# Kernel optimization log

Hardware: AMD Instinct MI355X
Metric: run time of the kernel (lower is better)

Reference implementation:

```python
import jax, jax.numpy as jnp
import numpy as np

B, T, D = 2, 2048, 2048
H = 8
DK = 256   # head_qk_dim
DV = 512   # head_v_dim
C = 64     # retention chunk size
EPS = 1e-5
ROPE_BASE = 10000.0


def _rotary(x):
    # x: [B, T, H, DK], non-interleaved (rotate-half) rotary over full head dim
    half = DK // 2
    inv_freq = 1.0 / (ROPE_BASE ** (jnp.arange(0, DK, 2, dtype=jnp.float32) / DK))
    freqs = jnp.arange(T, dtype=jnp.float32)[:, None] * inv_freq[None, :]  # [T, half]
    cos = jnp.cos(freqs)[None, :, None, :].astype(x.dtype)
    sin = jnp.sin(freqs)[None, :, None, :].astype(x.dtype)
    x1, x2 = x[..., :half], x[..., half:]
    return jnp.concatenate([x1 * cos - x2 * sin, x2 * cos + x1 * sin], axis=-1)


def setup_inputs() -> dict:
    key = jax.random.key(0)
    ks = jax.random.split(key, 6)
    s = 2.0 ** (-2.5) * (2.0 / 2048.0) ** 0.5  # xavier_uniform-ish scale, gain 2^-2.5
    return {
        "hidden_states": jax.random.normal(ks[0], (B, T, D), jnp.float32),
        "Wq": jax.random.normal(ks[1], (H * DK, D), jnp.float32) * s,
        "Wk": jax.random.normal(ks[2], (H * DK, D), jnp.float32) * s,
        "Wv": jax.random.normal(ks[3], (H * DV, D), jnp.float32) * s,
        "Wg": jax.random.normal(ks[4], (H * DV, D), jnp.float32) * s,
        "Wo": jax.random.normal(ks[5], (D, H * DV), jnp.float32) * s,
        "g_norm_weight": jnp.ones((DV,), jnp.float32),
    }


def reference(hidden_states, Wq, Wk, Wv, Wg, Wo, g_norm_weight):
    x = hidden_states  # [B, T, D]
    q = (x @ Wq.T).reshape(B, T, H, DK)
    k = (x @ Wk.T).reshape(B, T, H, DK)
    q = _rotary(q)
    k = _rotary(k)
    q = q.transpose(0, 2, 1, 3) * (DK ** -0.5)        # [B, H, T, DK]
    k = k.transpose(0, 2, 1, 3)                       # [B, H, T, DK]
    v = (x @ Wv.T).reshape(B, T, H, DV).transpose(0, 2, 1, 3)  # [B, H, T, DV]

    # RetNet multi-scale per-head decay
    logb = jnp.log(1.0 - 2.0 ** (-5.0 - jnp.arange(H, dtype=jnp.float32)))  # [H]
    i = jnp.arange(C, dtype=jnp.float32)
    # intra-chunk decay mask b^{i-j} for i>=j: [H, C, C]
    Dmask = jnp.where(i[:, None] >= i[None, :],
                      jnp.exp(logb[:, None, None] * (i[:, None] - i[None, :])), 0.0)
    q_dec = jnp.exp(logb[:, None] * (i + 1.0))        # [H, C]  decay applied to q vs carried state
    k_dec = jnp.exp(logb[:, None] * (C - 1.0 - i))    # [H, C]  decay applied to k for state update
    chunk_dec = jnp.exp(logb * C)                     # [H]

    N = T // C
    qc = q.reshape(B, H, N, C, DK).transpose(2, 0, 1, 3, 4)  # [N, B, H, C, DK]
    kc = k.reshape(B, H, N, C, DK).transpose(2, 0, 1, 3, 4)
    vc = v.reshape(B, H, N, C, DV).transpose(2, 0, 1, 3, 4)

    def body(S, inp):
        qi, ki, vi = inp  # [B,H,C,DK], [B,H,C,DK], [B,H,C,DV]
        inter = jnp.einsum('bhcd,bhdv->bhcv', qi * q_dec[None, :, :, None], S)
        scores = jnp.einsum('bhcd,bhmd->bhcm', qi, ki) * Dmask[None]
        o = inter + jnp.einsum('bhcm,bhmv->bhcv', scores, vi)
        S_new = S * chunk_dec[None, :, None, None] + \
                jnp.einsum('bhcd,bhcv->bhdv', ki * k_dec[None, :, :, None], vi)
        return S_new, o

    S0 = jnp.zeros((B, H, DK, DV), x.dtype)
    _, oc = jax.lax.scan(body, S0, (qc, kc, vc))  # oc: [N, B, H, C, DV]
    o = oc.transpose(1, 2, 0, 3, 4).reshape(B, H, T, DV).transpose(0, 2, 1, 3)  # [B, T, H, DV]

    g = (x @ Wg.T).reshape(B, T, H, DV)
    # fused RMSNorm + swish gate (per head_v_dim)
    o_n = o * jax.lax.rsqrt(jnp.mean(o * o, axis=-1, keepdims=True) + EPS) * g_norm_weight
    o = o_n * (g * jax.nn.sigmoid(g))
    return o.reshape(B, T, H * DV) @ Wo.T  # [B, T, D]
```

## Files before the change

### kernel.cpp

```cpp
#include <hip/hip_runtime.h>


typedef unsigned short u16;
typedef unsigned int u32;
typedef short bf16x8 __attribute__((ext_vector_type(8)));
typedef short s16x4 __attribute__((ext_vector_type(4)));
typedef float f32x4 __attribute__((ext_vector_type(4)));
typedef u32 u32x2 __attribute__((ext_vector_type(2)));
typedef u32 u32x4 __attribute__((ext_vector_type(4)));

typedef __attribute__((address_space(3))) u32 lds_u32;
typedef __attribute__((address_space(1))) const u32 gbl_u32;

__device__ __forceinline__ float bf2f(u16 u) {
    union { u32 i; float f; } x; x.i = ((u32)u) << 16; return x.f;
}
__device__ __forceinline__ u16 f2bf(float f) {
    union { float f; u32 i; } x; x.f = f;
    u32 u = x.i;
    u += 0x7fffu + ((u >> 16) & 1u);
    return (u16)(u >> 16);
}
__device__ __forceinline__ f32x4 mfma16(bf16x8 a, bf16x8 b, f32x4 c) {
    return __builtin_amdgcn_mfma_f32_16x16x32_bf16(a, b, c, 0, 0, 0);
}
__device__ __forceinline__ void gload16(const u16* g, u16* lds) {
    __builtin_amdgcn_global_load_lds((gbl_u32*)(unsigned long long)g,
                                     (lds_u32*)(u32)(unsigned long long)lds, 16, 0, 0);
}

__global__ __launch_bounds__(256)
void cvt_bf16(const float* __restrict__ src, u16* __restrict__ dst)
{
    size_t i = ((size_t)blockIdx.x * 256 + threadIdx.x) * 8;
    f32x4 a = *(const f32x4*)(src + i);
    f32x4 b = *(const f32x4*)(src + i + 4);
    bf16x8 r;
#pragma unroll
    for (int j = 0; j < 4; j++) { r[j] = (short)f2bf(a[j]); r[j + 4] = (short)f2bf(b[j]); }
    *(bf16x8*)(dst + i) = r;
}

template<bool CF32>
__global__ __launch_bounds__(256, 2)
void gemm_bt(const u16* __restrict__ A, const u16* __restrict__ Bm,
             void* __restrict__ Cv, int N, int K)
{
    __shared__ u16 Ab[128 * 64];
    __shared__ u16 Bb[128 * 64];
    const int tid = threadIdx.x;
    const int lane = tid & 63, wave = tid >> 6;
    const int quad = lane >> 4, l16 = lane & 15;
    const int tn = blockIdx.x, tm = blockIdx.y;
    const int wr = wave >> 1, wc = wave & 1;

    f32x4 acc[4][4];
#pragma unroll
    for (int i = 0; i < 4; i++)
#pragma unroll
        for (int j = 0; j < 4; j++) acc[i][j] = (f32x4){0.f, 0.f, 0.f, 0.f};

    const u16* Abase = A + (size_t)tm * 128 * K;
    const u16* Bbase = Bm + (size_t)tn * 128 * K;
    const int rsub = lane >> 3, csub = (lane & 7) * 8;

    for (int k0 = 0; k0 < K; k0 += 64) {
        __syncthreads();
#pragma unroll
        for (int i = 0; i < 4; i++) {
            int chunk = wave * 4 + i;
            int r = chunk * 8 + rsub;
            gload16(Abase + (size_t)r * K + k0 + csub, Ab + chunk * 512);
            gload16(Bbase + (size_t)r * K + k0 + csub, Bb + chunk * 512);
        }
        __syncthreads();
#pragma unroll
        for (int kc = 0; kc < 2; kc++) {
            bf16x8 af[4], bfr[4];
#pragma unroll
            for (int mt = 0; mt < 4; mt++)
                af[mt] = *(const bf16x8*)(Ab + (wr * 64 + mt * 16 + l16) * 64 + kc * 32 + quad * 8);
#pragma unroll
            for (int nt = 0; nt < 4; nt++)
                bfr[nt] = *(const bf16x8*)(Bb + (wc * 64 + nt * 16 + l16) * 64 + kc * 32 + quad * 8);
#pragma unroll
            for (int mt = 0; mt < 4; mt++)
#pragma unroll
                for (int nt = 0; nt < 4; nt++)
                    acc[mt][nt] = mfma16(af[mt], bfr[nt], acc[mt][nt]);
        }
    }
    const int row0 = tm * 128 + wr * 64 + quad * 4;
    const int col0 = tn * 128 + wc * 64 + l16;
#pragma unroll
    for (int mt = 0; mt < 4; mt++)
#pragma unroll
        for (int nt = 0; nt < 4; nt++)
#pragma unroll
            for (int r = 0; r < 4; r++) {
                size_t idx = (size_t)(row0 + mt * 16 + r) * N + col0 + nt * 16;
                if constexpr (CF32) ((float*)Cv)[idx] = acc[mt][nt][r];
                else                ((u16*)Cv)[idx]   = f2bf(acc[mt][nt][r]);
            }
}

__global__ __launch_bounds__(256, 2)
void rotary_scores(u16* __restrict__ q, const u16* __restrict__ k,
                   u16* __restrict__ kT, u16* __restrict__ P)
{
    __shared__ u16 qS[64 * 264];
    __shared__ u16 kS[64 * 264];
    const int tid = threadIdx.x;
    const int lane = tid & 63, wave = tid >> 6;
    const int quad = lane >> 4, l16 = lane & 15;
    const int bx = blockIdx.x;
    const int bh = bx & 15, n = bx >> 4;
    const int b = bh >> 3, h = bh & 7;
    const int t0 = n * 64;

    const int row = tid >> 2;
    const int j0 = (tid & 3) * 32;
    const size_t rowbase = (size_t)(b * 2048 + t0 + row) * 2048 + h * 256;
    const float tpos = (float)(t0 + row);
#pragma unroll
    for (int i = 0; i < 4; i++) {
        int j = j0 + i * 8;
        bf16x8 x1 = *(const bf16x8*)(q + rowbase + j);
        bf16x8 x2 = *(const bf16x8*)(q + rowbase + j + 128);
        bf16x8 y1 = *(const bf16x8*)(k + rowbase + j);
        bf16x8 y2 = *(const bf16x8*)(k + rowbase + j + 128);
        bf16x8 o1, o2, p1, p2;
#pragma unroll
        for (int e = 0; e < 8; e++) {
            float inv = expf((-9.210340371976184f / 128.f) * (float)(j + e));
            float ang = tpos * inv;
            float sv = sinf(ang), cv = cosf(ang);
            float a = bf2f((u16)x1[e]), bb = bf2f((u16)x2[e]);
            o1[e] = (short)f2bf((a * cv - bb * sv) * 0.0625f);
            o2[e] = (short)f2bf((bb * cv + a * sv) * 0.0625f);
            float e1 = bf2f((u16)y1[e]), e2 = bf2f((u16)y2[e]);
            p1[e] = (short)f2bf(e1 * cv - e2 * sv);
            p2[e] = (short)f2bf(e2 * cv + e1 * sv);
        }
        *(bf16x8*)(q + rowbase + j)       = o1;
        *(bf16x8*)(q + rowbase + j + 128) = o2;
        *(bf16x8*)(qS + row * 264 + j)       = o1;
        *(bf16x8*)(qS + row * 264 + j + 128) = o2;
        *(bf16x8*)(kS + row * 264 + j)       = p1;
        *(bf16x8*)(kS + row * 264 + j + 128) = p2;
    }
    __syncthreads();

    const float logb = logf(1.0f - exp2f(-5.0f - (float)h));
    f32x4 sc[4];
#pragma unroll
    for (int i = 0; i < 4; i++) sc[i] = (f32x4){0.f, 0.f, 0.f, 0.f};
#pragma unroll
    for (int kc = 0; kc < 8; kc++) {
        bf16x8 af = *(const bf16x8*)(qS + (wave * 16 + l16) * 264 + kc * 32 + quad * 8);
#pragma unroll
        for (int mt = 0; mt < 4; mt++) {
            bf16x8 bk = *(const bf16x8*)(kS + (mt * 16 + l16) * 264 + kc * 32 + quad * 8);
            sc[mt] = mfma16(af, bk, sc[mt]);
        }
    }
    u16* Pb = P + ((size_t)(bh * 32 + n)) * 64 * 64;
#pragma unroll
    for (int r = 0; r < 4; r++) {
        int cr = wave * 16 + quad * 4 + r;
        float rowe = __expf(logb * (float)(cr - 63));
#pragma unroll
        for (int mt = 0; mt < 4; mt++) {
            int m = mt * 16 + l16;
            float val = (cr >= m) ? sc[mt][r] * rowe : 0.0f;
            Pb[cr * 64 + m] = f2bf(val);
        }
    }

    const int d = tid;
    u16* dst = kT + ((size_t)(bh * 256 + d)) * 2048 + t0;
#pragma unroll
    for (int g8 = 0; g8 < 8; g8++) {
        bf16x8 w;
#pragma unroll
        for (int e = 0; e < 8; e++) w[e] = (short)kS[(g8 * 8 + e) * 264 + d];
        *(bf16x8*)(dst + g8 * 8) = w;
    }
}

__global__ __launch_bounds__(512, 2)
void retention(const u16* __restrict__ Q, const u16* __restrict__ KT,
               const u16* __restrict__ V, const u16* __restrict__ P,
               u16* __restrict__ O)
{
    __shared__ u16 St[32 * 264];
    __shared__ u16 vsT[32 * 72];

    const int tid = threadIdx.x;
    const int lane = tid & 63, wave = tid >> 6;
    const int quad = lane >> 4, l16 = lane & 15;
    const int bx = blockIdx.x;
    const int bh = bx & 15, vt = bx >> 4;
    const int b = bh >> 3, h = bh & 7;
    const int cgrp = wave >> 1, vhalf = wave & 1;

    const float logb = logf(1.0f - exp2f(-5.0f - (float)h));
    const float cdec = __expf(logb * 64.0f);

    int cr[4];
    float qdecr[4];
#pragma unroll
    for (int r = 0; r < 4; r++) {
        cr[r] = cgrp * 16 + quad * 4 + r;
        qdecr[r] = __expf(logb * (float)(cr[r] + 1));
    }
    const int mv = tid >> 3;
    const int vc4 = (tid & 7) * 4;
    const float kdv = __expf(logb * (float)(63 - mv));

    for (int i = tid; i < 32 * 264; i += 512) St[i] = 0;

    f32x4 Sacc[2][2];
#pragma unroll
    for (int dt = 0; dt < 2; dt++)
#pragma unroll
        for (int nt = 0; nt < 2; nt++) Sacc[dt][nt] = (f32x4){0.f, 0.f, 0.f, 0.f};

    for (int n = 0; n < 32; n++) {
        const int t0 = n * 64;
        u32x2 vv = *(const u32x2*)(V + (size_t)(b * 2048 + t0 + mv) * 4096 + h * 512 + vt * 32 + vc4);
        bf16x8 qf[8];
#pragma unroll
        for (int kc = 0; kc < 8; kc++)
            qf[kc] = *(const bf16x8*)(Q + (size_t)(b * 2048 + t0 + cgrp * 16 + l16) * 2048
                                      + h * 256 + kc * 32 + quad * 8);
        bf16x8 ktf[2][2];
#pragma unroll
        for (int dt = 0; dt < 2; dt++)
#pragma unroll
            for (int kc2 = 0; kc2 < 2; kc2++)
                ktf[dt][kc2] = *(const bf16x8*)(KT + (size_t)(bh * 256 + wave * 32 + dt * 16 + l16) * 2048
                                                + t0 + kc2 * 32 + quad * 8);
        bf16x8 pf[2];
#pragma unroll
        for (int kc2 = 0; kc2 < 2; kc2++)
            pf[kc2] = *(const bf16x8*)(P + ((size_t)(bh * 32 + n) * 64 + cgrp * 16 + l16) * 64
                                       + kc2 * 32 + quad * 8);

        __syncthreads();

        {
            u16 e0 = (u16)(vv[0] & 0xffff), e1 = (u16)(vv[0] >> 16);
            u16 e2 = (u16)(vv[1] & 0xffff), e3 = (u16)(vv[1] >> 16);
            vsT[(vc4 + 0) * 72 + mv] = f2bf(bf2f(e0) * kdv);
            vsT[(vc4 + 1) * 72 + mv] = f2bf(bf2f(e1) * kdv);
            vsT[(vc4 + 2) * 72 + mv] = f2bf(bf2f(e2) * kdv);
            vsT[(vc4 + 3) * 72 + mv] = f2bf(bf2f(e3) * kdv);
        }
        f32x4 oacc = (f32x4){0.f, 0.f, 0.f, 0.f};
#pragma unroll
        for (int kc = 0; kc < 8; kc++) {
            bf16x8 bs = *(const bf16x8*)(St + (vhalf * 16 + l16) * 264 + kc * 32 + quad * 8);
            oacc = mfma16(qf[kc], bs, oacc);
        }

        __syncthreads();

#pragma unroll
        for (int dt = 0; dt < 2; dt++)
#pragma unroll
            for (int nt = 0; nt < 2; nt++)
#pragma unroll
                for (int e = 0; e < 4; e++) Sacc[dt][nt][e] *= cdec;
#pragma unroll
        for (int kc2 = 0; kc2 < 2; kc2++) {
            bf16x8 bv0 = *(const bf16x8*)(vsT + l16 * 72 + kc2 * 32 + quad * 8);
            bf16x8 bv1 = *(const bf16x8*)(vsT + (16 + l16) * 72 + kc2 * 32 + quad * 8);
#pragma unroll
            for (int dt = 0; dt < 2; dt++) {
                Sacc[dt][0] = mfma16(ktf[dt][kc2], bv0, Sacc[dt][0]);
                Sacc[dt][1] = mfma16(ktf[dt][kc2], bv1, Sacc[dt][1]);
            }
        }
#pragma unroll
        for (int r = 0; r < 4; r++) oacc[r] *= qdecr[r];
#pragma unroll
        for (int kc2 = 0; kc2 < 2; kc2++) {
            bf16x8 bv = *(const bf16x8*)(vsT + (vhalf * 16 + l16) * 72 + kc2 * 32 + quad * 8);
            oacc = mfma16(pf[kc2], bv, oacc);
        }
#pragma unroll
        for (int r = 0; r < 4; r++)
            O[(size_t)(b * 2048 + t0 + cr[r]) * 4096 + h * 512 + vt * 32 + vhalf * 16 + l16] =
                f2bf(oacc[r]);
#pragma unroll
        for (int dt = 0; dt < 2; dt++)
#pragma unroll
            for (int nt = 0; nt < 2; nt++) {
                s16x4 w;
#pragma unroll
                for (int r = 0; r < 4; r++) w[r] = (short)f2bf(Sacc[dt][nt][r]);
                *(s16x4*)(St + (nt * 16 + l16) * 264 + wave * 32 + dt * 16 + quad * 4) = w;
            }
    }
}

__global__ __launch_bounds__(256)
void norm_gate(const u16* __restrict__ O, const u16* __restrict__ G,
               const float* __restrict__ gw, u16* __restrict__ ON)
{
    const int lane = threadIdx.x & 63;
    const size_t row = (size_t)blockIdx.x * 4 + (threadIdx.x >> 6);
    bf16x8 ov = *(const bf16x8*)(O + row * 512 + lane * 8);
    bf16x8 gv = *(const bf16x8*)(G + row * 512 + lane * 8);
    f32x4 w0 = *(const f32x4*)(gw + lane * 8);
    f32x4 w1 = *(const f32x4*)(gw + lane * 8 + 4);
    float of[8], gf[8];
    float ss = 0.f;
#pragma unroll
    for (int j = 0; j < 8; j++) {
        of[j] = bf2f((u16)ov[j]);
        gf[j] = bf2f((u16)gv[j]);
        ss += of[j] * of[j];
    }
#pragma unroll
    for (int off = 32; off > 0; off >>= 1) ss += __shfl_down(ss, off);
    ss = __shfl(ss, 0);
    const float rms = rsqrtf(ss * (1.0f / 512.0f) + 1e-5f);
    bf16x8 res;
#pragma unroll
    for (int j = 0; j < 8; j++) {
        float wj = (j < 4) ? w0[j] : w1[j - 4];
        float xn = of[j] * rms * wj;
        float sg = gf[j] / (1.f + __expf(-gf[j]));
        res[j] = (short)f2bf(xn * sg);
    }
    *(bf16x8*)(ON + row * 512 + lane * 8) = res;
}

extern "C" void kernel_launch(void* const* d_in, const int* in_sizes, int n_in,
                              void* d_out, int out_size, void* d_ws, size_t ws_size,
                              hipStream_t stream)
{
    const float* x  = (const float*)d_in[0];
    const float* Wq = (const float*)d_in[1];
    const float* Wk = (const float*)d_in[2];
    const float* Wv = (const float*)d_in[3];
    const float* Wg = (const float*)d_in[4];
    const float* Wo = (const float*)d_in[5];
    const float* gw = (const float*)d_in[6];
    float* out = (float*)d_out;

    const size_t M8 = (size_t)4096 * 2048;
    u16* Pb = (u16*)d_ws;
    u16* q  = Pb + (size_t)16 * 32 * 64 * 64;
    u16* k  = q + M8;
    u16* kT = k + M8;
    u16* v  = kT + M8;
    u16* o  = v + 2 * M8;
    u16* xb = o + 2 * M8;
    u16* g  = q;
    u16* on = v;
    u16* wt = kT;

    dim3 blk(256, 1, 1), blk512(512, 1, 1);
    cvt_bf16<<<dim3(4096, 1, 1), blk, 0, stream>>>(x, xb);

    cvt_bf16<<<dim3(2048, 1, 1), blk, 0, stream>>>(Wq, wt);
    gemm_bt<false><<<dim3(16, 32, 1), blk, 0, stream>>>(xb, wt, q, 2048, 2048);
    cvt_bf16<<<dim3(2048, 1, 1), blk, 0, stream>>>(Wk, wt);
    gemm_bt<false><<<dim3(16, 32, 1), blk, 0, stream>>>(xb, wt, k, 2048, 2048);
    cvt_bf16<<<dim3(4096, 1, 1), blk, 0, stream>>>(Wv, wt);
    gemm_bt<false><<<dim3(32, 32, 1), blk, 0, stream>>>(xb, wt, v, 4096, 2048);

    rotary_scores<<<dim3(512, 1, 1), blk, 0, stream>>>(q, k, kT, Pb);
    retention<<<dim3(256, 1, 1), blk512, 0, stream>>>(q, kT, v, Pb, o);

    cvt_bf16<<<dim3(4096, 1, 1), blk, 0, stream>>>(Wg, kT);
    gemm_bt<false><<<dim3(32, 32, 1), blk, 0, stream>>>(xb, kT, g, 4096, 2048);
    norm_gate<<<dim3(8192, 1, 1), blk, 0, stream>>>(o, g, gw, on);
    cvt_bf16<<<dim3(4096, 1, 1), blk, 0, stream>>>(Wo, kT);
    gemm_bt<true><<<dim3(16, 32, 1), blk, 0, stream>>>(on, kT, out, 2048, 4096);
}
```

Measured before the change: 695.0 us.

## Split retention kernel over 16-wide value tiles to double grid parallelism

The retention kernel now gives each block a 16-column slice of the value dimension instead of 32, so the grid grows from 256 to 512 blocks and fills more of the GPU's compute units. Only four of the eight waves compute outputs, while all eight keep updating the carried state. The next chunk's V load is prefetched across iterations, and __syncthreads is replaced by a custom LDS waitcnt plus barrier. In exchange, Q, K^T and P loads are duplicated across twice as many blocks and half the waves sit idle during the output phase.

```diff
diff --git a/kernel.cpp b/kernel.cpp
--- a/kernel.cpp
+++ b/kernel.cpp
@@ -27,6 +27,9 @@
 __device__ __forceinline__ void gload16(const u16* g, u16* lds) {
     __builtin_amdgcn_global_load_lds((gbl_u32*)(unsigned long long)g,
                                      (lds_u32*)(u32)(unsigned long long)lds, 16, 0, 0);
+}
+__device__ __forceinline__ void bar_lds() {
+    __asm__ volatile("s_waitcnt lgkmcnt(0)\n\ts_barrier" ::: "memory");
 }
 
 __global__ __launch_bounds__(256)
@@ -193,8 +196,8 @@
                const u16* __restrict__ V, const u16* __restrict__ P,
                u16* __restrict__ O)
 {
-    __shared__ u16 St[32 * 264];
-    __shared__ u16 vsT[32 * 72];
+    __shared__ u16 St[16 * 264];
+    __shared__ u16 vsT[16 * 72];
 
     const int tid = threadIdx.x;
     const int lane = tid & 63, wave = tid >> 6;
@@ -202,7 +205,6 @@
     const int bx = blockIdx.x;
     const int bh = bx & 15, vt = bx >> 4;
     const int b = bh >> 3, h = bh & 7;
-    const int cgrp = wave >> 1, vhalf = wave & 1;
 
     const float logb = logf(1.0f - exp2f(-5.0f - (float)h));
     const float cdec = __expf(logb * 64.0f);
@@ -211,29 +213,35 @@
     float qdecr[4];
 #pragma unroll
     for (int r = 0; r < 4; r++) {
-        cr[r] = cgrp * 16 + quad * 4 + r;
+        cr[r] = wave * 16 + quad * 4 + r;
         qdecr[r] = __expf(logb * (float)(cr[r] + 1));
     }
     const int mv = tid >> 3;
-    const int vc4 = (tid & 7) * 4;
+    const int vc2 = (tid & 7) * 2;
     const float kdv = __expf(logb * (float)(63 - mv));
 
-    for (int i = tid; i < 32 * 264; i += 512) St[i] = 0;
-
-    f32x4 Sacc[2][2];
-#pragma unroll
-    for (int dt = 0; dt < 2; dt++)
-#pragma unroll
-        for (int nt = 0; nt < 2; nt++) Sacc[dt][nt] = (f32x4){0.f, 0.f, 0.f, 0.f};
+    for (int i = tid; i < 16 * 264; i += 512) St[i] = 0;
+
+    f32x4 Sacc[2];
+    Sacc[0] = (f32x4){0.f, 0.f, 0.f, 0.f};
+    Sacc[1] = (f32x4){0.f, 0.f, 0.f, 0.f};
+
+    const u16* vptr0 = V + (size_t)(b * 2048 + mv) * 4096 + h * 512 + vt * 16 + vc2;
+    u32 vv = *(const u32*)vptr0;
 
     for (int n = 0; n < 32; n++) {
         const int t0 = n * 64;
-        u32x2 vv = *(const u32x2*)(V + (size_t)(b * 2048 + t0 + mv) * 4096 + h * 512 + vt * 32 + vc4);
-        bf16x8 qf[8];
-#pragma unroll
-        for (int kc = 0; kc < 8; kc++)
-            qf[kc] = *(const bf16x8*)(Q + (size_t)(b * 2048 + t0 + cgrp * 16 + l16) * 2048
-                                      + h * 256 + kc * 32 + quad * 8);
+        bf16x8 qf[8], pf[2];
+        if (wave < 4) {
+#pragma unroll
+            for (int kc = 0; kc < 8; kc++)
+                qf[kc] = *(const bf16x8*)(Q + (size_t)(b * 2048 + t0 + wave * 16 + l16) * 2048
+                                          + h * 256 + kc * 32 + quad * 8);
+#pragma unroll
+            for (int kc2 = 0; kc2 < 2; kc2++)
+                pf[kc2] = *(const bf16x8*)(P + ((size_t)(bh * 32 + n) * 64 + wave * 16 + l16) * 64
+                                           + kc2 * 32 + quad * 8);
+        }
         bf16x8 ktf[2][2];
 #pragma unroll
         for (int dt = 0; dt < 2; dt++)
@@ -241,67 +249,55 @@
             for (int kc2 = 0; kc2 < 2; kc2++)
                 ktf[dt][kc2] = *(const bf16x8*)(KT + (size_t)(bh * 256 + wave * 32 + dt * 16 + l16) * 2048
                                                 + t0 + kc2 * 32 + quad * 8);
-        bf16x8 pf[2];
-#pragma unroll
-        for (int kc2 = 0; kc2 < 2; kc2++)
-            pf[kc2] = *(const bf16x8*)(P + ((size_t)(bh * 32 + n) * 64 + cgrp * 16 + l16) * 64
-                                       + kc2 * 32 + quad * 8);
-
-        __syncthreads();
-
-        {
-            u16 e0 = (u16)(vv[0] & 0xffff), e1 = (u16)(vv[0] >> 16);
-            u16 e2 = (u16)(vv[1] & 0xffff), e3 = (u16)(vv[1] >> 16);
-            vsT[(vc4 + 0) * 72 + mv] = f2bf(bf2f(e0) * kdv);
-            vsT[(vc4 + 1) * 72 + mv] = f2bf(bf2f(e1) * kdv);
-            vsT[(vc4 + 2) * 72 + mv] = f2bf(bf2f(e2) * kdv);
-            vsT[(vc4 + 3) * 72 + mv] = f2bf(bf2f(e3) * kdv);
-        }
+
+        bar_lds();
+
+        vsT[(vc2 + 0) * 72 + mv] = f2bf(bf2f((u16)(vv & 0xffff)) * kdv);
+        vsT[(vc2 + 1) * 72 + mv] = f2bf(bf2f((u16)(vv >> 16)) * kdv);
+        if (n < 31) vv = *(const u32*)(vptr0 + (size_t)(t0 + 64) * 4096);
+
         f32x4 oacc = (f32x4){0.f, 0.f, 0.f, 0.f};
-#pragma unroll
-        for (int kc = 0; kc < 8; kc++) {
-            bf16x8 bs = *(const bf16x8*)(St + (vhalf * 16 + l16) * 264 + kc * 32 + quad * 8);
-            oacc = mfma16(qf[kc], bs, oacc);
-        }
-
-        __syncthreads();
+        if (wave < 4) {
+#pragma unroll
+            for (int kc = 0; kc < 8; kc++) {
+                bf16x8 bs = *(const bf16x8*)(St + l16 * 264 + kc * 32 + quad * 8);
+                oacc = mfma16(qf[kc], bs, oacc);
+            }
+        }
+
+        bar_lds();
 
 #pragma unroll
         for (int dt = 0; dt < 2; dt++)
 #pragma unroll
-            for (int nt = 0; nt < 2; nt++)
-#pragma unroll
-                for (int e = 0; e < 4; e++) Sacc[dt][nt][e] *= cdec;
+            for (int e = 0; e < 4; e++) Sacc[dt][e] *= cdec;
 #pragma unroll
         for (int kc2 = 0; kc2 < 2; kc2++) {
-            bf16x8 bv0 = *(const bf16x8*)(vsT + l16 * 72 + kc2 * 32 + quad * 8);
-            bf16x8 bv1 = *(const bf16x8*)(vsT + (16 + l16) * 72 + kc2 * 32 + quad * 8);
-#pragma unroll
-            for (int dt = 0; dt < 2; dt++) {
-                Sacc[dt][0] = mfma16(ktf[dt][kc2], bv0, Sacc[dt][0]);
-                Sacc[dt][1] = mfma16(ktf[dt][kc2], bv1, Sacc[dt][1]);
+            bf16x8 bv = *(const bf16x8*)(vsT + l16 * 72 + kc2 * 32 + quad * 8);
+#pragma unroll
+            for (int dt = 0; dt < 2; dt++)
+                Sacc[dt] = mfma16(ktf[dt][kc2], bv, Sacc[dt]);
+        }
+        if (wave < 4) {
+#pragma unroll
+            for (int r = 0; r < 4; r++) oacc[r] *= qdecr[r];
+#pragma unroll
+            for (int kc2 = 0; kc2 < 2; kc2++) {
+                bf16x8 bv = *(const bf16x8*)(vsT + l16 * 72 + kc2 * 32 + quad * 8);
+                oacc = mfma16(pf[kc2], bv, oacc);
             }
-        }
-#pragma unroll
-        for (int r = 0; r < 4; r++) oacc[r] *= qdecr[r];
-#pragma unroll
-        for (int kc2 = 0; kc2 < 2; kc2++) {
-            bf16x8 bv = *(const bf16x8*)(vsT + (vhalf * 16 + l16) * 72 + kc2 * 32 + quad * 8);
-            oacc = mfma16(pf[kc2], bv, oacc);
-        }
-#pragma unroll
-        for (int r = 0; r < 4; r++)
-            O[(size_t)(b * 2048 + t0 + cr[r]) * 4096 + h * 512 + vt * 32 + vhalf * 16 + l16] =
-                f2bf(oacc[r]);
-#pragma unroll
-        for (int dt = 0; dt < 2; dt++)
-#pragma unroll
-            for (int nt = 0; nt < 2; nt++) {
-                s16x4 w;
-#pragma unroll
-                for (int r = 0; r < 4; r++) w[r] = (short)f2bf(Sacc[dt][nt][r]);
-                *(s16x4*)(St + (nt * 16 + l16) * 264 + wave * 32 + dt * 16 + quad * 4) = w;
-            }
+#pragma unroll
+            for (int r = 0; r < 4; r++)
+                O[(size_t)(b * 2048 + t0 + cr[r]) * 4096 + h * 512 + vt * 16 + l16] =
+                    f2bf(oacc[r]);
+        }
+#pragma unroll
+        for (int dt = 0; dt < 2; dt++) {
+            s16x4 w;
+#pragma unroll
+            for (int r = 0; r < 4; r++) w[r] = (short)f2bf(Sacc[dt][r]);
+            *(s16x4*)(St + l16 * 264 + wave * 32 + dt * 16 + quad * 4) = w;
+        }
     }
 }
 
@@ -374,7 +370,7 @@
     gemm_bt<false><<<dim3(32, 32, 1), blk, 0, stream>>>(xb, wt, v, 4096, 2048);
 
     rotary_scores<<<dim3(512, 1, 1), blk, 0, stream>>>(q, k, kT, Pb);
-    retention<<<dim3(256, 1, 1), blk512, 0, stream>>>(q, kT, v, Pb, o);
+    retention<<<dim3(512, 1, 1), blk512, 0, stream>>>(q, kT, v, Pb, o);
 
     cvt_bf16<<<dim3(4096, 1, 1), blk, 0, stream>>>(Wg, kT);
     gemm_bt<false><<<dim3(32, 32, 1), blk, 0, stream>>>(xb, kT, g, 4096, 2048);
```

New measurement: 717.6 us. 1.03x slower.
